# Kernel optimization log

Hardware: AMD Instinct MI355X
Metric: run time of the kernel (lower is better)

Reference implementation:

```python
import jax, jax.numpy as jnp
import numpy as np

DIM = 256
R = 2
D = DIM // R  # 128
M = 19
BS = 16384
EPS = 1e-5


def setup_inputs() -> dict:
    key = jax.random.key(0)
    ks = jax.random.split(key, 12)
    s = 0.02
    return {
        "x": jax.random.normal(ks[0], (BS, M * DIM), dtype=jnp.float32),
        "g": jax.random.normal(ks[1], (BS, M * DIM), dtype=jnp.float32),
        # fc = Linear(dim,d) -> ReLU -> BatchNorm1d(d) -> Linear(d,d)
        "W1": jax.random.normal(ks[2], (D, DIM), dtype=jnp.float32) * s,
        "b1": jnp.zeros((D,), dtype=jnp.float32),
        "gamma": jnp.ones((D,), dtype=jnp.float32),
        "beta": jnp.zeros((D,), dtype=jnp.float32),
        "W2": jax.random.normal(ks[3], (D, D), dtype=jnp.float32) * s,
        "b2": jnp.zeros((D,), dtype=jnp.float32),
        # 19 branch Linears stacked: fcs Linear(d,d), g_fcs Linear(dim+d, dim)
        "Wf": jax.random.normal(ks[4], (M, D, D), dtype=jnp.float32) * s,
        "bf": jnp.zeros((M, D), dtype=jnp.float32),
        "Wg": jax.random.normal(ks[5], (M, DIM, D + DIM), dtype=jnp.float32) * s,
        "bg": jnp.zeros((M, DIM), dtype=jnp.float32),
    }


def reference(x, g, W1, b1, gamma, beta, W2, b2, Wf, bf, Wg, bg):
    bs = x.shape[0]
    x3 = x.reshape(bs, M, -1)  # [bs, 19, dim]
    g3 = g.reshape(bs, M, -1)  # [bs, 19, dim]

    fea_u = jnp.sum(x3, axis=1)  # [bs, dim]
    h = jax.nn.relu(fea_u @ W1.T + b1)  # [bs, d]
    # BatchNorm1d (training mode: batch statistics, biased variance)
    mu = jnp.mean(h, axis=0)
    var = jnp.var(h, axis=0)
    h = (h - mu) * jax.lax.rsqrt(var + EPS) * gamma + beta
    fea_z = h @ W2.T + b2  # [bs, d]

    # all 19 branch fcs in one batched GEMM: [bs, 19, d]
    v = jnp.einsum('bd,mkd->bmk', fea_z, Wf) + bf
    cat = jnp.concatenate([v, g3], axis=2)  # [bs, 19, d+dim]
    att = jnp.einsum('bmk,mok->bmo', cat, Wg) + bg  # [bs, 19, dim]
    att = jax.nn.softmax(att, axis=1)  # softmax over the 19 branches

    fea_v = jnp.sum(x3 * att, axis=1)  # [bs, dim]
    return fea_v
```

## Files before the change

kernel.cpp:

```cpp
#include <hip/hip_runtime.h>
#include <math.h>

#define BSZ 16384
#define MB  19
#define KIN 4864

typedef __attribute__((ext_vector_type(8))) short short8;
typedef __attribute__((ext_vector_type(4))) float float4v;

static __device__ inline unsigned short f2bf(float f) {
  union { float f; unsigned u; } c; c.f = f;
  unsigned r = c.u + 0x7FFF + ((c.u >> 16) & 1);
  return (unsigned short)(r >> 16);
}

__global__ __launch_bounds__(256) void kw_w1b(const float* __restrict__ W1,
                                              unsigned short* __restrict__ W1b) {
  int i = blockIdx.x * 256 + threadIdx.x;
  W1b[i] = f2bf(W1[i]);
}

__global__ __launch_bounds__(128) void kp_combine(
    const float* __restrict__ Wg, const float* __restrict__ Wf,
    const float* __restrict__ bf, const float* __restrict__ bg,
    unsigned short* __restrict__ Wall, float* __restrict__ bc) {
  int mo = blockIdx.x;
  int m = mo >> 8;
  int d = threadIdx.x;
  __shared__ float wg_s[128];
  wg_s[d] = Wg[(size_t)mo * 384 + d];
  __syncthreads();
  float acc = 0.f;
  for (int k = 0; k < 128; ++k)
    acc = fmaf(wg_s[k], Wf[(m * 128 + k) * 128 + d], acc);
  unsigned short* wr = Wall + (size_t)mo * 384;
  wr[d]       = f2bf(acc);
  wr[128 + d] = f2bf(Wg[(size_t)mo * 384 + 128 + d]);
  wr[256 + d] = f2bf(Wg[(size_t)mo * 384 + 256 + d]);
  if (d == 0) {
    float b = bg[mo];
    for (int k = 0; k < 128; ++k) b = fmaf(wg_s[k], bf[m * 128 + k], b);
    bc[mo] = b;
  }
}

__global__ __launch_bounds__(512) void k1_mfma(
    const float* __restrict__ x, const unsigned short* __restrict__ W1b,
    const float* __restrict__ b1, unsigned short* __restrict__ h_pre,
    float* __restrict__ gsum, float* __restrict__ gsq) {
  __shared__ unsigned short fuB[32][272];
  __shared__ float bs[128], bq[128];
  const int t = threadIdx.x, b0 = blockIdx.x * 32;
  const int w = t >> 6, l = t & 63;

#pragma unroll
  for (int i = 0; i < 4; ++i) {
    int r = w * 4 + i;
    const float* xr = x + (size_t)(b0 + r) * KIN + l * 4;
    float4 s = {0.f, 0.f, 0.f, 0.f};
    for (int m = 0; m < MB; ++m) {
      float4 v = *(const float4*)(xr + m * 256);
      s.x += v.x; s.y += v.y; s.z += v.z; s.w += v.w;
    }
    ushort4 u;
    u.x = f2bf(s.x); u.y = f2bf(s.y); u.z = f2bf(s.z); u.w = f2bf(s.w);
    *(ushort4*)&fuB[r][l * 4] = u;
  }
  if (t < 128) { bs[t] = 0.f; bq[t] = 0.f; }
  __syncthreads();

  const int col = l & 15, q = l >> 4;
  const int d = w * 16 + col;
  float bv = b1[d];
  float4v acc0 = {bv, bv, bv, bv}, acc1 = {bv, bv, bv, bv};
#pragma unroll
  for (int ks = 0; ks < 8; ++ks) {
    short8 a0 = *(const short8*)&fuB[col][ks * 32 + q * 8];
    short8 a1 = *(const short8*)&fuB[16 + col][ks * 32 + q * 8];
    short8 b  = *(const short8*)(W1b + d * 256 + ks * 32 + q * 8);
    acc0 = __builtin_amdgcn_mfma_f32_16x16x32_bf16(a0, b, acc0, 0, 0, 0);
    acc1 = __builtin_amdgcn_mfma_f32_16x16x32_bf16(a1, b, acc1, 0, 0, 0);
  }
  float s = 0.f, qq = 0.f;
#pragma unroll
  for (int j = 0; j < 4; ++j) {
    float v0 = fmaxf(acc0[j], 0.f);
    float v1 = fmaxf(acc1[j], 0.f);
    h_pre[(size_t)(b0 + q * 4 + j) * 128 + d]      = f2bf(v0);
    h_pre[(size_t)(b0 + 16 + q * 4 + j) * 128 + d] = f2bf(v1);
    s += v0 + v1; qq = fmaf(v0, v0, qq); qq = fmaf(v1, v1, qq);
  }
  atomicAdd(&bs[d], s);
  atomicAdd(&bq[d], qq);
  __syncthreads();
  if (t < 128) { atomicAdd(&gsum[t], bs[t]); atomicAdd(&gsq[t], bq[t]); }
}

__global__ __launch_bounds__(128) void k2b_finalize(
    const float* __restrict__ gsum, const float* __restrict__ gsq,
    const float* __restrict__ gamma, const float* __restrict__ beta,
    const float* __restrict__ W2, const float* __restrict__ b2,
    unsigned short* __restrict__ W2s, float* __restrict__ b2s) {
  __shared__ float sc[128], sh[128];
  int d = threadIdx.x;
  float mu  = gsum[d] * (1.f / BSZ);
  float var = gsq[d]  * (1.f / BSZ) - mu * mu;
  float s   = gamma[d] * rsqrtf(var + 1e-5f);
  sc[d] = s;
  sh[d] = beta[d] - mu * s;
  __syncthreads();
  float acc = b2[d];
  for (int k = 0; k < 128; ++k) {
    float w2 = W2[d * 128 + k];
    W2s[d * 128 + k] = f2bf(w2 * sc[k]);
    acc = fmaf(w2, sh[k], acc);
  }
  b2s[d] = acc;
}

__global__ __launch_bounds__(512, 4) void k3_fused(
    const float* __restrict__ x, const float* __restrict__ g,
    const unsigned short* __restrict__ h_pre,
    const unsigned short* __restrict__ W2s, const float* __restrict__ b2s,
    const unsigned short* __restrict__ Wall, const float* __restrict__ bc,
    float* __restrict__ out) {
  __shared__ unsigned short fz[32][144];
  __shared__ unsigned short gb[2][32][272];
  __shared__ float att[32][260];
  const int t = threadIdx.x, b0 = blockIdx.x * 32;
  const int w = t >> 6, l = t & 63;
  const int col = l & 15, q = l >> 4;

  {
    const int d = w * 16 + col;
    float bv = b2s[d];
    float4v a2_0 = {bv, bv, bv, bv}, a2_1 = {bv, bv, bv, bv};
#pragma unroll
    for (int ks = 0; ks < 4; ++ks) {
      short8 A0 = *(const short8*)(h_pre + (size_t)(b0 + col) * 128 + ks * 32 + q * 8);
      short8 A1 = *(const short8*)(h_pre + (size_t)(b0 + 16 + col) * 128 + ks * 32 + q * 8);
      short8 B  = *(const short8*)(W2s + d * 128 + ks * 32 + q * 8);
      a2_0 = __builtin_amdgcn_mfma_f32_16x16x32_bf16(A0, B, a2_0, 0, 0, 0);
      a2_1 = __builtin_amdgcn_mfma_f32_16x16x32_bf16(A1, B, a2_1, 0, 0, 0);
    }
#pragma unroll
    for (int j = 0; j < 4; ++j) {
      fz[q * 4 + j][d]      = f2bf(a2_0[j]);
      fz[16 + q * 4 + j][d] = f2bf(a2_1[j]);
    }
  }
#pragma unroll
  for (int i = 0; i < 4; ++i) {
    int r = i * 8 + w;
    float4 gv = *(const float4*)(g + (size_t)(b0 + r) * KIN + l * 4);
    ushort4 u;
    u.x = f2bf(gv.x); u.y = f2bf(gv.y); u.z = f2bf(gv.z); u.w = f2bf(gv.w);
    *(ushort4*)&gb[0][r][l * 4] = u;
  }
  __syncthreads();

  float4v Ov[4], Sm[4];
#pragma unroll
  for (int u = 0; u < 4; ++u) { Ov[u] = float4v{0,0,0,0}; Sm[u] = float4v{0,0,0,0}; }

  const int o0 = w * 32;
  const int mr = t >> 4, mc = t & 15;

  for (int m = 0; m < MB; ++m) {
    const int p = m & 1;
    float bc0 = bc[m * 256 + o0 + col];
    float bc1 = bc[m * 256 + o0 + 16 + col];
    float4v acc[4];
    acc[0] = float4v{bc0, bc0, bc0, bc0};
    acc[1] = float4v{bc1, bc1, bc1, bc1};
    acc[2] = float4v{bc0, bc0, bc0, bc0};
    acc[3] = float4v{bc1, bc1, bc1, bc1};
    const unsigned short* wb0 = Wall + (size_t)(m * 256 + o0 + col) * 384;
    const unsigned short* wb1 = wb0 + (size_t)16 * 384;
#pragma unroll
    for (int ks = 0; ks < 12; ++ks) {
      short8 a0, a1;
      if (ks < 4) {
        a0 = *(const short8*)&fz[col][ks * 32 + q * 8];
        a1 = *(const short8*)&fz[16 + col][ks * 32 + q * 8];
      } else {
        a0 = *(const short8*)&gb[p][col][(ks - 4) * 32 + q * 8];
        a1 = *(const short8*)&gb[p][16 + col][(ks - 4) * 32 + q * 8];
      }
      short8 b0v = *(const short8*)(wb0 + ks * 32 + q * 8);
      short8 b1v = *(const short8*)(wb1 + ks * 32 + q * 8);
      acc[0] = __builtin_amdgcn_mfma_f32_16x16x32_bf16(a0, b0v, acc[0], 0, 0, 0);
      acc[1] = __builtin_amdgcn_mfma_f32_16x16x32_bf16(a0, b1v, acc[1], 0, 0, 0);
      acc[2] = __builtin_amdgcn_mfma_f32_16x16x32_bf16(a1, b0v, acc[2], 0, 0, 0);
      acc[3] = __builtin_amdgcn_mfma_f32_16x16x32_bf16(a1, b1v, acc[3], 0, 0, 0);
    }
#pragma unroll
    for (int rt = 0; rt < 2; ++rt) {
#pragma unroll
      for (int j = 0; j < 4; ++j) {
        int row = rt * 16 + q * 4 + j;
        att[row][o0 + col]      = __expf(acc[rt * 2 + 0][j]);
        att[row][o0 + 16 + col] = __expf(acc[rt * 2 + 1][j]);
      }
    }
    __syncthreads();

    {
      const float* xr = x + (size_t)(b0 + mr) * KIN + m * 256 + mc * 4;
#pragma unroll
      for (int u = 0; u < 4; ++u) {
        float4 xv = *(const float4*)(xr + u * 64);
        float4 ev = *(const float4*)&att[mr][mc * 4 + u * 64];
        Sm[u][0] += ev.x; Sm[u][1] += ev.y; Sm[u][2] += ev.z; Sm[u][3] += ev.w;
        Ov[u][0] = fmaf(ev.x, xv.x, Ov[u][0]);
        Ov[u][1] = fmaf(ev.y, xv.y, Ov[u][1]);
        Ov[u][2] = fmaf(ev.z, xv.z, Ov[u][2]);
        Ov[u][3] = fmaf(ev.w, xv.w, Ov[u][3]);
      }
    }
    if (m + 1 < MB) {
#pragma unroll
      for (int i = 0; i < 4; ++i) {
        int r = i * 8 + w;
        float4 gv = *(const float4*)(g + (size_t)(b0 + r) * KIN + (m + 1) * 256 + l * 4);
        ushort4 u;
        u.x = f2bf(gv.x); u.y = f2bf(gv.y); u.z = f2bf(gv.z); u.w = f2bf(gv.w);
        *(ushort4*)&gb[1 - p][r][l * 4] = u;
      }
    }
    __syncthreads();
  }

#pragma unroll
  for (int u = 0; u < 4; ++u) {
    float4 o4;
    o4.x = Ov[u][0] / Sm[u][0];
    o4.y = Ov[u][1] / Sm[u][1];
    o4.z = Ov[u][2] / Sm[u][2];
    o4.w = Ov[u][3] / Sm[u][3];
    *(float4*)(out + (size_t)(b0 + mr) * 256 + mc * 4 + u * 64) = o4;
  }
}

extern "C" void kernel_launch(void* const* d_in, const int* in_sizes, int n_in,
                              void* d_out, int out_size, void* d_ws, size_t ws_size,
                              hipStream_t stream) {
  const float* x     = (const float*)d_in[0];
  const float* g     = (const float*)d_in[1];
  const float* W1    = (const float*)d_in[2];
  const float* b1    = (const float*)d_in[3];
  const float* gamma = (const float*)d_in[4];
  const float* beta  = (const float*)d_in[5];
  const float* W2    = (const float*)d_in[6];
  const float* b2    = (const float*)d_in[7];
  const float* Wf    = (const float*)d_in[8];
  const float* bf    = (const float*)d_in[9];
  const float* Wg    = (const float*)d_in[10];
  const float* bg    = (const float*)d_in[11];
  float* out = (float*)d_out;

  float* ws = (float*)d_ws;
  float* gsum = ws;
  float* gsq  = gsum + 128;
  float* bc   = gsq + 128;
  float* b2s  = bc + MB * 256;
  unsigned short* Wall = (unsigned short*)(b2s + 128);
  unsigned short* W1b  = Wall + (size_t)MB * 256 * 384;
  unsigned short* W2s  = W1b + 128 * 256;
  unsigned short* h_pre = W2s + 128 * 128;

  hipMemsetAsync(gsum, 0, 256 * sizeof(float), stream);
  kw_w1b<<<128, 256, 0, stream>>>(W1, W1b);
  kp_combine<<<MB * 256, 128, 0, stream>>>(Wg, Wf, bf, bg, Wall, bc);
  k1_mfma<<<BSZ / 32, 512, 0, stream>>>(x, W1b, b1, h_pre, gsum, gsq);
  k2b_finalize<<<1, 128, 0, stream>>>(gsum, gsq, gamma, beta, W2, b2, W2s, b2s);
  k3_fused<<<BSZ / 32, 512, 0, stream>>>(x, g, h_pre, W2s, b2s, Wall, bc, out);
}
```

Before: 878.2 us.

## Prefetch x and g into registers ahead of use and use LDS-only barriers

Loads of x for the next branch and g for two branches ahead are issued into registers at the end of each iteration, so their global-memory latency overlaps the following MFMA work instead of stalling right before use. The __syncthreads calls are replaced with a barrier that waits only on LDS counters (lgkmcnt), so outstanding global loads are not drained at each barrier. This costs extra registers for the prefetched float4s and depends on the hand-written waitcnt being enough to keep LDS accesses correct.

```diff
diff --git a/kernel.cpp b/kernel.cpp
--- a/kernel.cpp
+++ b/kernel.cpp
@@ -12,6 +12,12 @@
   union { float f; unsigned u; } c; c.f = f;
   unsigned r = c.u + 0x7FFF + ((c.u >> 16) & 1);
   return (unsigned short)(r >> 16);
+}
+
+static __device__ inline void bar_lgkm() {
+  asm volatile("s_waitcnt lgkmcnt(0)" ::: "memory");
+  __builtin_amdgcn_s_barrier();
+  asm volatile("" ::: "memory");
 }
 
 __global__ __launch_bounds__(256) void kw_w1b(const float* __restrict__ W1,
@@ -157,14 +163,26 @@
     u.x = f2bf(gv.x); u.y = f2bf(gv.y); u.z = f2bf(gv.z); u.w = f2bf(gv.w);
     *(ushort4*)&gb[0][r][l * 4] = u;
   }
-  __syncthreads();
-
-  float4v Ov[4], Sm[4];
-#pragma unroll
-  for (int u = 0; u < 4; ++u) { Ov[u] = float4v{0,0,0,0}; Sm[u] = float4v{0,0,0,0}; }
 
   const int o0 = w * 32;
   const int mr = t >> 4, mc = t & 15;
+
+  float4 Xr[4], Gr[4];
+  {
+    const float* xr = x + (size_t)(b0 + mr) * KIN + mc * 4;
+#pragma unroll
+    for (int u = 0; u < 4; ++u) Xr[u] = *(const float4*)(xr + u * 64);
+#pragma unroll
+    for (int i = 0; i < 4; ++i) {
+      int r = i * 8 + w;
+      Gr[i] = *(const float4*)(g + (size_t)(b0 + r) * KIN + 256 + l * 4);
+    }
+  }
+  __syncthreads();
+
+  float4v Ov[4], Sm[4];
+#pragma unroll
+  for (int u = 0; u < 4; ++u) { Ov[u] = float4v{0,0,0,0}; Sm[u] = float4v{0,0,0,0}; }
 
   for (int m = 0; m < MB; ++m) {
     const int p = m & 1;
@@ -203,32 +221,40 @@
         att[row][o0 + 16 + col] = __expf(acc[rt * 2 + 1][j]);
       }
     }
-    __syncthreads();
-
-    {
-      const float* xr = x + (size_t)(b0 + mr) * KIN + m * 256 + mc * 4;
-#pragma unroll
-      for (int u = 0; u < 4; ++u) {
-        float4 xv = *(const float4*)(xr + u * 64);
-        float4 ev = *(const float4*)&att[mr][mc * 4 + u * 64];
-        Sm[u][0] += ev.x; Sm[u][1] += ev.y; Sm[u][2] += ev.z; Sm[u][3] += ev.w;
-        Ov[u][0] = fmaf(ev.x, xv.x, Ov[u][0]);
-        Ov[u][1] = fmaf(ev.y, xv.y, Ov[u][1]);
-        Ov[u][2] = fmaf(ev.z, xv.z, Ov[u][2]);
-        Ov[u][3] = fmaf(ev.w, xv.w, Ov[u][3]);
-      }
-    }
+    bar_lgkm();
+
     if (m + 1 < MB) {
 #pragma unroll
       for (int i = 0; i < 4; ++i) {
         int r = i * 8 + w;
-        float4 gv = *(const float4*)(g + (size_t)(b0 + r) * KIN + (m + 1) * 256 + l * 4);
-        ushort4 u;
-        u.x = f2bf(gv.x); u.y = f2bf(gv.y); u.z = f2bf(gv.z); u.w = f2bf(gv.w);
-        *(ushort4*)&gb[1 - p][r][l * 4] = u;
+        ushort4 u4;
+        u4.x = f2bf(Gr[i].x); u4.y = f2bf(Gr[i].y);
+        u4.z = f2bf(Gr[i].z); u4.w = f2bf(Gr[i].w);
+        *(ushort4*)&gb[1 - p][r][l * 4] = u4;
       }
     }
-    __syncthreads();
+#pragma unroll
+    for (int u = 0; u < 4; ++u) {
+      float4 ev = *(const float4*)&att[mr][mc * 4 + u * 64];
+      Sm[u][0] += ev.x; Sm[u][1] += ev.y; Sm[u][2] += ev.z; Sm[u][3] += ev.w;
+      Ov[u][0] = fmaf(ev.x, Xr[u].x, Ov[u][0]);
+      Ov[u][1] = fmaf(ev.y, Xr[u].y, Ov[u][1]);
+      Ov[u][2] = fmaf(ev.z, Xr[u].z, Ov[u][2]);
+      Ov[u][3] = fmaf(ev.w, Xr[u].w, Ov[u][3]);
+    }
+    if (m + 1 < MB) {
+      const float* xr = x + (size_t)(b0 + mr) * KIN + (m + 1) * 256 + mc * 4;
+#pragma unroll
+      for (int u = 0; u < 4; ++u) Xr[u] = *(const float4*)(xr + u * 64);
+    }
+    if (m + 2 < MB) {
+#pragma unroll
+      for (int i = 0; i < 4; ++i) {
+        int r = i * 8 + w;
+        Gr[i] = *(const float4*)(g + (size_t)(b0 + r) * KIN + (m + 2) * 256 + l * 4);
+      }
+    }
+    bar_lgkm();
   }
 
 #pragma unroll
```

After: 914.2 us. 1.04x slower.
